# Kernel optimization log

Hardware: AMD Instinct MI355X
Metric: run time of the kernel (lower is better)

Reference implementation:

```python
import jax, jax.numpy as jnp
import numpy as np

NT, NP, E, H, DIM = 100000, 50000, 800000, 128, 128


def _lin(key, fi, fo):
    k1, k2 = jax.random.split(key)
    w = jax.random.normal(k1, (fi, fo), jnp.float32) * 0.02
    b = jax.random.normal(k2, (fo,), jnp.float32) * 0.02
    return w, b


def _conv_params(key, d_src, d_dst, d_out):
    ks = jax.random.split(key, 5)
    Wq, bq = _lin(ks[0], d_dst, d_out)
    Wk, bk = _lin(ks[1], d_src, d_out)
    Wv, bv = _lin(ks[2], d_src, d_out)
    Ws, bs = _lin(ks[3], d_dst, d_out)
    Wb = jax.random.normal(ks[4], (3 * d_out, 1), jnp.float32) * 0.02
    return Wq, bq, Wk, bk, Wv, bv, Ws, bs, Wb


def setup_inputs() -> dict:
    key = jax.random.key(0)
    ks = jax.random.split(key, 12)
    inp = {}
    inp['x_token'] = jax.random.normal(ks[0], (NT, 1), jnp.float32)
    inp['x_phrase'] = jax.random.normal(ks[1], (NP, H), jnp.float32)
    inp['W_emb'], inp['b_emb'] = _lin(ks[2], 1, H)
    (inp['Wq_tp'], inp['bq_tp'], inp['Wk_tp'], inp['bk_tp'], inp['Wv_tp'],
     inp['bv_tp'], inp['Ws_tp'], inp['bs_tp'], inp['Wb_tp']) = _conv_params(ks[3], H, H, H)
    (inp['Wq_pt'], inp['bq_pt'], inp['Wk_pt'], inp['bk_pt'], inp['Wv_pt'],
     inp['bv_pt'], inp['Ws_pt'], inp['bs_pt'], inp['Wb_pt']) = _conv_params(ks[4], H, H, H)
    inp['W_head'], inp['b_head'] = _lin(ks[5], H, DIM)
    inp['src_tp'] = jax.random.randint(ks[6], (E,), 0, NT, jnp.int32)
    inp['dst_tp'] = jax.random.randint(ks[7], (E,), 0, NP, jnp.int32)
    inp['src_pt'] = jax.random.randint(ks[8], (E,), 0, NP, jnp.int32)
    inp['dst_pt'] = jax.random.randint(ks[9], (E,), 0, NT, jnp.int32)
    return inp


def _tconv(x_src, x_dst, src, dst, Wq, bq, Wk, bk, Wv, bv, Ws, bs, Wb):
    # PyG TransformerConv, heads=1, beta=True, eval mode (no dropout).
    n_dst = x_dst.shape[0]
    d = Wq.shape[1]
    q = x_dst @ Wq + bq          # [Ndst, d]
    k = x_src @ Wk + bk          # [Nsrc, d]
    v = x_src @ Wv + bv          # [Nsrc, d]
    scores = jnp.sum(q[dst] * k[src], axis=-1) / jnp.sqrt(jnp.float32(d))  # [E]
    m = jax.ops.segment_max(scores, dst, num_segments=n_dst)
    m = jnp.where(jnp.isfinite(m), m, 0.0)  # nodes with no in-edges
    e = jnp.exp(scores - m[dst])
    denom = jax.ops.segment_sum(e, dst, num_segments=n_dst)
    alpha = e / (denom[dst] + 1e-16)                       # segment softmax over dst
    out = jax.ops.segment_sum(alpha[:, None] * v[src], dst, num_segments=n_dst)
    skip = x_dst @ Ws + bs
    beta = jax.nn.sigmoid(jnp.concatenate([out, skip, out - skip], axis=-1) @ Wb)
    return beta * skip + (1.0 - beta) * out


def _forward(x_token, x_phrase, W_emb, b_emb,
             Wq_tp, bq_tp, Wk_tp, bk_tp, Wv_tp, bv_tp, Ws_tp, bs_tp, Wb_tp,
             Wq_pt, bq_pt, Wk_pt, bk_pt, Wv_pt, bv_pt, Ws_pt, bs_pt, Wb_pt,
             W_head, b_head, src_tp, dst_tp, src_pt, dst_pt):
    h_t = x_token @ W_emb + b_emb   # [NT, H]
    h_p = x_phrase                  # [NP, H]
    # conv1 (HeteroConv aggr='sum'; each node type has exactly one incoming edge type)
    p1 = _tconv(h_t, h_p, src_tp, dst_tp, Wq_tp, bq_tp, Wk_tp, bk_tp, Wv_tp, bv_tp, Ws_tp, bs_tp, Wb_tp)
    t1 = _tconv(h_p, h_t, src_pt, dst_pt, Wq_pt, bq_pt, Wk_pt, bk_pt, Wv_pt, bv_pt, Ws_pt, bs_pt, Wb_pt)
    p1 = jax.nn.leaky_relu(p1, 0.01)
    t1 = jax.nn.leaky_relu(t1, 0.01)
    # conv2 shares the SAME conv modules (same params). Only the token output is used downstream.
    t2 = _tconv(p1, t1, src_pt, dst_pt, Wq_pt, bq_pt, Wk_pt, bk_pt, Wv_pt, bv_pt, Ws_pt, bs_pt, Wb_pt)
    return t2 @ W_head + b_head     # [NT, DIM]


def reference(x_token, x_phrase, W_emb, b_emb, Wq_tp, bq_tp, Wk_tp, bk_tp, Wv_tp, bv_tp, Ws_tp, bs_tp, Wb_tp, Wq_pt, bq_pt, Wk_pt, bk_pt, Wv_pt, bv_pt, Ws_pt, bs_pt, Wb_pt, W_head, b_head, src_tp, dst_tp, src_pt, dst_pt):
    return _forward(x_token, x_phrase, W_emb, b_emb,
                    Wq_tp, bq_tp, Wk_tp, bk_tp, Wv_tp, bv_tp, Ws_tp, bs_tp, Wb_tp,
                    Wq_pt, bq_pt, Wk_pt, bk_pt, Wv_pt, bv_pt, Ws_pt, bs_pt, Wb_pt,
                    W_head, b_head, src_tp, dst_tp, src_pt, dst_pt)
```

## Files before the change

kernel.cpp:

```cpp
#include <hip/hip_runtime.h>
#include <math.h>

#define NT 100000
#define NP 50000
#define NE 800000
#define H 128
#define NB 196
#define BCAP 8192

#define CDIV(a,b) (((a)+(b)-1)/(b))

typedef __attribute__((ext_vector_type(8))) short s16x8;
typedef __attribute__((ext_vector_type(4))) short s16x4;
typedef __attribute__((ext_vector_type(4))) unsigned short u16x4;
typedef __attribute__((ext_vector_type(4))) float f32x4;

static __device__ __forceinline__ float dot4(float4 a, float4 b){
  return a.x*b.x + a.y*b.y + a.z*b.z + a.w*b.w;
}
static __device__ __forceinline__ float b2f(unsigned short u){
  union { unsigned int i; float f; } c; c.i = ((unsigned int)u) << 16; return c.f;
}
static __device__ __forceinline__ unsigned short f2b(float f){
  union { float f; unsigned int i; } c; c.f = f;
  unsigned int x = c.i;
  unsigned int r = (x + 0x7fffu + ((x >> 16) & 1u)) >> 16;
  return (unsigned short)r;
}
static __device__ __forceinline__ float4 cvt4u(u16x4 h){
  return make_float4(b2f(h[0]), b2f(h[1]), b2f(h[2]), b2f(h[3]));
}

__global__ void kvec4(const float* __restrict__ e, const float* __restrict__ be,
    const float* W0, const float* bi0, float* u0, float* w0,
    const float* W1, const float* bi1, float* u1, float* w1,
    const float* W2, const float* bi2, float* u2, float* w2,
    const float* W3, const float* bi3, float* u3, float* w3){
  const float *W, *bi; float *u, *w;
  switch (blockIdx.x){
    case 0: W=W0; bi=bi0; u=u0; w=w0; break;
    case 1: W=W1; bi=bi1; u=u1; w=w1; break;
    case 2: W=W2; bi=bi2; u=u2; w=w2; break;
    default:W=W3; bi=bi3; u=u3; w=w3; break;
  }
  int j = threadIdx.x;
  float su = 0.f, sw = 0.f;
  for (int i = 0; i < H; ++i) {
    float wv = W[i*H + j];
    su += e[i]*wv;
    sw += be[i]*wv;
  }
  u[j] = su;
  w[j] = sw + bi[j];
}

__global__ void ksetup(const float* __restrict__ Wq, const float* __restrict__ Wk,
                       const float* __restrict__ bq, float* __restrict__ Wqk,
                       float* __restrict__ bqk){
  int i = blockIdx.x;
  int m = threadIdx.x;
  __shared__ float wqr[H];
  wqr[m] = Wq[i*H + m];
  __syncthreads();
  const float* wkr = Wk + m*H;
  float s = 0.f;
  for (int j = 0; j < H; ++j) s += wqr[j] * wkr[j];
  Wqk[i*H + m] = s;
  if (i == 0){
    float t = 0.f;
    for (int j = 0; j < H; ++j) t += bq[j] * wkr[j];
    bqk[m] = t;
  }
}
__global__ void kvqb(const float* __restrict__ Wq, const float* __restrict__ bq,
                     const float* __restrict__ bk, float* __restrict__ vqb,
                     float* __restrict__ c0){
  int i = threadIdx.x;
  float s = 0.f;
  for (int j = 0; j < H; ++j) s += Wq[i*H + j]*bk[j];
  vqb[i] = s;
  if (i == 0){
    float t = 0.f;
    for (int j = 0; j < H; ++j) t += bq[j]*bk[j];
    *c0 = t;
  }
}

__global__ void kprep(const float* W0, unsigned short* P0,
                      const float* W1, unsigned short* P1,
                      const float* W2, unsigned short* P2,
                      const float* W3, unsigned short* P3,
                      const float* W4, unsigned short* P4,
                      const float* W5, unsigned short* P5,
                      const float* W6, unsigned short* P6){
  const float* W; unsigned short* P;
  switch (blockIdx.x){
    case 0: W=W0; P=P0; break;
    case 1: W=W1; P=P1; break;
    case 2: W=W2; P=P2; break;
    case 3: W=W3; P=P3; break;
    case 4: W=W4; P=P4; break;
    case 5: W=W5; P=P5; break;
    default:W=W6; P=P6; break;
  }
  int tid = threadIdx.x;
  for (int it = 0; it < 16; ++it){
    int gid = it*256 + tid;
    int n  = gid & 127;
    int kg = gid >> 7;
    int k0 = kg*4;
    float w0 = W[(k0+0)*H + n];
    float w1 = W[(k0+1)*H + n];
    float w2 = W[(k0+2)*H + n];
    float w3 = W[(k0+3)*H + n];
    unsigned short h0=f2b(w0), h1=f2b(w1), h2=f2b(w2), h3=f2b(w3);
    s16x4 hv; hv[0]=(short)h0; hv[1]=(short)h1; hv[2]=(short)h2; hv[3]=(short)h3;
    s16x4 lv; lv[0]=(short)f2b(w0-b2f(h0)); lv[1]=(short)f2b(w1-b2f(h1));
              lv[2]=(short)f2b(w2-b2f(h2)); lv[3]=(short)f2b(w3-b2f(h3));
    int base = n*128 + (((kg>>1) ^ (n&15))<<3) + ((kg&1)<<2);
    *(s16x4*)(P + base) = hv;
    *(s16x4*)(P + 16384 + base) = lv;
  }
}

static __device__ __forceinline__ void stage_pre(const unsigned short* __restrict__ Wpre,
    unsigned short* __restrict__ WHL, int tid){
  const s16x8* src = (const s16x8*)Wpre;
  #pragma unroll
  for (int c = 0; c < 2; ++c){
    s16x8 tmp[8];
    #pragma unroll
    for (int it = 0; it < 8; ++it) tmp[it] = src[(c*8+it)*256 + tid];
    #pragma unroll
    for (int it = 0; it < 8; ++it) *(s16x8*)(WHL + ((c*8+it)*256 + tid)*8) = tmp[it];
  }
}
static __device__ __forceinline__ void stage_pre32(const unsigned short* __restrict__ Wpre,
    unsigned short* __restrict__ WH, int tid){
  const s16x8* src = (const s16x8*)Wpre;
  s16x8 tmp[8];
  #pragma unroll
  for (int it = 0; it < 8; ++it) tmp[it] = src[it*256 + tid];
  #pragma unroll
  for (int it = 0; it < 8; ++it) *(s16x8*)(WH + (it*256 + tid)*8) = tmp[it];
}

template<bool USE_AL>
static __device__ __forceinline__ void mfma_pass(const s16x8 AH[2][4], const s16x8 AL[2][4],
    const unsigned short* __restrict__ WH, const unsigned short* __restrict__ WL,
    int l15, int l4, f32x4 acc[2][8]){
  #pragma unroll
  for (int g = 0; g < 2; ++g)
    #pragma unroll
    for (int t = 0; t < 8; ++t){ acc[g][t][0]=0.f; acc[g][t][1]=0.f; acc[g][t][2]=0.f; acc[g][t][3]=0.f; }
  #pragma unroll
  for (int s = 0; s < 4; ++s){
    #pragma unroll
    for (int t = 0; t < 8; ++t){
      int n = t*16 + l15;
      int off = n*128 + (((s*4 + l4) ^ l15)<<3);
      s16x8 BH = *(const s16x8*)(WH + off);
      s16x8 BL = *(const s16x8*)(WL + off);
      #pragma unroll
      for (int g = 0; g < 2; ++g){
        acc[g][t] = __builtin_amdgcn_mfma_f32_16x16x32_bf16(AH[g][s], BH, acc[g][t], 0,0,0);
        acc[g][t] = __builtin_amdgcn_mfma_f32_16x16x32_bf16(AH[g][s], BL, acc[g][t], 0,0,0);
        if constexpr (USE_AL)
          acc[g][t] = __builtin_amdgcn_mfma_f32_16x16x32_bf16(AL[g][s], BH, acc[g][t], 0,0,0);
      }
    }
  }
}
static __device__ __forceinline__ void mfma_pass1(const s16x8 AH[2][4],
    const unsigned short* __restrict__ WH, int l15, int l4, f32x4 acc[2][8]){
  #pragma unroll
  for (int g = 0; g < 2; ++g)
    #pragma unroll
    for (int t = 0; t < 8; ++t){ acc[g][t][0]=0.f; acc[g][t][1]=0.f; acc[g][t][2]=0.f; acc[g][t][3]=0.f; }
  #pragma unroll
  for (int s = 0; s < 4; ++s){
    #pragma unroll
    for (int t = 0; t < 8; ++t){
      int n = t*16 + l15;
      int off = n*128 + (((s*4 + l4) ^ l15)<<3);
      s16x8 BH = *(const s16x8*)(WH + off);
      #pragma unroll
      for (int g = 0; g < 2; ++g)
        acc[g][t] = __builtin_amdgcn_mfma_f32_16x16x32_bf16(AH[g][s], BH, acc[g][t], 0,0,0);
    }
  }
}

static __device__ __forceinline__ void load_a_f32(const float* __restrict__ X, int M,
    int row0, int w, int l15, int l4, s16x8 AH[2][4], s16x8 AL[2][4]){
  #pragma unroll
  for (int g = 0; g < 2; ++g){
    int row = row0 + w*32 + g*16 + l15;
    const float* xr = X + (size_t)row*H;
    bool ok = row < M;
    #pragma unroll
    for (int s = 0; s < 4; ++s){
      int kb = s*32 + l4*8;
      float4 f0 = ok ? *(const float4*)(xr+kb)   : make_float4(0.f,0.f,0.f,0.f);
      float4 f1 = ok ? *(const float4*)(xr+kb+4) : make_float4(0.f,0.f,0.f,0.f);
      float xs[8] = {f0.x,f0.y,f0.z,f0.w,f1.x,f1.y,f1.z,f1.w};
      s16x8 h, lo;
      #pragma unroll
      for (int e = 0; e < 8; ++e){
        unsigned short hh = f2b(xs[e]);
        h[e]  = (short)hh;
        lo[e] = (short)f2b(xs[e] - b2f(hh));
      }
      AH[g][s] = h; AL[g][s] = lo;
    }
  }
}
static __device__ __forceinline__ void load_a_bf16(const unsigned short* __restrict__ Xb, int M,
    int row0, int w, int l15, int l4, s16x8 AH[2][4]){
  #pragma unroll
  for (int g = 0; g < 2; ++g){
    int row = row0 + w*32 + g*16 + l15;
    const unsigned short* xr = Xb + (size_t)row*H;
    bool ok = row < M;
    #pragma unroll
    for (int s = 0; s < 4; ++s){
      s16x8 h = {0,0,0,0,0,0,0,0};
      if (ok) h = *(const s16x8*)(xr + s*32 + l4*8);
      AH[g][s] = h;
    }
  }
}

static __device__ __forceinline__ void dots_epi(const f32x4 (&acc)[2][8],
    const float* __restrict__ bias, const float* __restrict__ uvec,
    const float* __restrict__ wvec, float2* __restrict__ acout,
    int row0, int M, int w, int l15, int l4){
  float ub[8], wb[8], bb[8];
  #pragma unroll
  for (int t=0;t<8;++t){ ub[t]=uvec[t*16+l15]; wb[t]=wvec[t*16+l15]; bb[t]=bias[t*16+l15]; }
  #pragma unroll
  for (int g=0; g<2; ++g){
    #pragma unroll
    for (int r=0;r<4;++r){
      float pa=0.f, pc=0.f;
      #pragma unroll
      for (int t=0;t<8;++t){ float y=acc[g][t][r]+bb[t]; pa+=y*ub[t]; pc+=y*wb[t]; }
      #pragma unroll
      for (int o=1;o<16;o<<=1){ pa+=__shfl_xor(pa,o); pc+=__shfl_xor(pc,o); }
      int row=row0+w*32+g*16+l4*4+r;
      if (l15==0 && row<M) acout[row]=make_float2(pa,pc);
    }
  }
}

static __device__ __forceinline__ void store_c_bf16(unsigned short* __restrict__ Y, int ld, int of,
    const f32x4 (&acc)[2][8], const float* __restrict__ bias,
    int row0, int M, int w, int l15, int l4){
  float bb[8];
  #pragma unroll
  for (int t=0;t<8;++t) bb[t]=bias[t*16+l15];
  #pragma unroll
  for (int g=0; g<2; ++g){
    #pragma unroll
    for (int r=0;r<4;++r){
      int row = row0 + w*32 + g*16 + l4*4 + r;
      if (row < M){
        unsigned short* dr = Y + (size_t)row*ld + of;
        #pragma unroll
        for (int t=0;t<8;++t) dr[t*16+l15] = f2b(acc[g][t][r] + bb[t]);
      }
    }
  }
}
static __device__ __forceinline__ void store_c_f32(float* __restrict__ Y,
    const f32x4 (&acc)[2][8], const float* __restrict__ bias,
    int row0, int M, int w, int l15, int l4){
  float bb[8];
  #pragma unroll
  for (int t=0;t<8;++t) bb[t]=bias[t*16+l15];
  #pragma unroll
  for (int g=0; g<2; ++g){
    #pragma unroll
    for (int r=0;r<4;++r){
      int row = row0 + w*32 + g*16 + l4*4 + r;
      if (row < M){
        float* dr = Y + (size_t)row*H;
        #pragma unroll
        for (int t=0;t<8;++t) dr[t*16+l15] = acc[g][t][r] + bb[t];
      }
    }
  }
}

__launch_bounds__(256)
__global__ void k_ph(const float* __restrict__ X, int M,
    const unsigned short* __restrict__ WqP, const float* __restrict__ bq,
    const float* __restrict__ uk, const float* __restrict__ wk, float2* __restrict__ ac1,
    const unsigned short* __restrict__ WsP, const float* __restrict__ bs, unsigned short* __restrict__ S1b,
    const unsigned short* __restrict__ WkP, const float* __restrict__ bk,
    const float* __restrict__ uq, const float* __restrict__ wq, float2* __restrict__ ac2,
    const unsigned short* __restrict__ WvP, const float* __restrict__ bv, unsigned short* __restrict__ Vb){
  __shared__ __align__(16) unsigned short WHL[32768];
  int tid=threadIdx.x, lane=tid&63, w=tid>>6, l15=lane&15, l4=lane>>4;
  int row0 = blockIdx.x*128;

  s16x8 AH[2][4], AL[2][4];
  load_a_f32(X, M, row0, w, l15, l4, AH, AL);

  f32x4 acc[2][8];
  stage_pre(WqP, WHL, tid); __syncthreads();
  mfma_pass<true>(AH, AL, WHL, WHL+16384, l15, l4, acc);
  __syncthreads();
  dots_epi(acc, bq, uk, wk, ac1, row0, M, w, l15, l4);

  stage_pre(WsP, WHL, tid); __syncthreads();
  mfma_pass<true>(AH, AL, WHL, WHL+16384, l15, l4, acc);
  __syncthreads();
  store_c_bf16(S1b, H, 0, acc, bs, row0, M, w, l15, l4);

  stage_pre(WkP, WHL, tid); __syncthreads();
  mfma_pass<true>(AH, AL, WHL, WHL+16384, l15, l4, acc);
  __syncthreads();
  dots_epi(acc, bk, uq, wq, ac2, row0, M, w, l15, l4);

  stage_pre(WvP, WHL, tid); __syncthreads();
  mfma_pass<true>(AH, AL, WHL, WHL+16384, l15, l4, acc);
  store_c_bf16(Vb, H, 0, acc, bv, row0, M, w, l15, l4);
}

__launch_bounds__(256)
__global__ void k_t3(const unsigned short* __restrict__ T1b, int M,
    const unsigned short* __restrict__ WqkP, const float* __restrict__ bqk,
    unsigned short* __restrict__ qkb,
    const float* __restrict__ vqb, const float* __restrict__ c0,
    float* __restrict__ qbf,
    const unsigned short* __restrict__ WsP, const float* __restrict__ bs,
    unsigned short* __restrict__ Sb){
  __shared__ __align__(16) unsigned short WH[16384];
  int tid=threadIdx.x, lane=tid&63, w=tid>>6, l15=lane&15, l4=lane>>4;
  int row0 = blockIdx.x*128;

  s16x8 AH[2][4];
  load_a_bf16(T1b, M, row0, w, l15, l4, AH);

  float cc0 = *c0;
  #pragma unroll
  for (int g = 0; g < 2; ++g){
    float p = 0.f;
    #pragma unroll
    for (int s = 0; s < 4; ++s){
      #pragma unroll
      for (int e = 0; e < 8; ++e)
        p += b2f((unsigned short)AH[g][s][e]) * vqb[s*32 + l4*8 + e];
    }
    p += __shfl_xor(p, 16);
    p += __shfl_xor(p, 32);
    int row = row0 + w*32 + g*16 + l15;
    if (l4 == 0 && row < M) qbf[row] = p + cc0;
  }

  f32x4 acc[2][8];
  stage_pre32(WqkP, WH, tid); __syncthreads();
  mfma_pass1(AH, WH, l15, l4, acc);
  __syncthreads();
  store_c_bf16(qkb, H, 0, acc, bqk, row0, M, w, l15, l4);

  stage_pre32(WsP, WH, tid); __syncthreads();
  mfma_pass1(AH, WH, l15, l4, acc);
  store_c_bf16(Sb, H, 0, acc, bs, row0, M, w, l15, l4);
}

__launch_bounds__(256)
__global__ void k_cmbh(const unsigned short* __restrict__ Opre, int M,
    const unsigned short* __restrict__ PV2, const float* __restrict__ bv,
    const unsigned short* __restrict__ Sb, const float* __restrict__ Wb,
    const int* __restrict__ deg,
    const unsigned short* __restrict__ PHD, const float* __restrict__ bh,
    float* __restrict__ out){
  __shared__ __align__(16) unsigned short WH[16384];
  __shared__ __align__(16) unsigned short SLDS[128][136];
  int tid=threadIdx.x, lane=tid&63, w=tid>>6, l15=lane&15, l4=lane>>4;
  int row0 = blockIdx.x*128;

  s16x8 AH[2][4];
  load_a_bf16(Opre, M, row0, w, l15, l4, AH);

  stage_pre32(PV2, WH, tid); __syncthreads();
  f32x4 acc[2][8];
  mfma_pass1(AH, WH, l15, l4, acc);

  {
    float bvv[8], wbA[8], wbB[8], wbC[8];
    #pragma unroll
    for (int t = 0; t < 8; ++t){
      int col = t*16 + l15;
      bvv[t] = bv[col];
      wbA[t] = Wb[col]; wbB[t] = Wb[H + col]; wbC[t] = Wb[2*H + col];
    }
    #pragma unroll
    for (int g = 0; g < 2; ++g){
      #pragma unroll
      for (int r = 0; r < 4; ++r){
        int rl = w*32 + g*16 + l4*4 + r;
        int row = row0 + rl;
        bool ok = row < M;
        float bsc = (ok && deg[row] > 0) ? 1.f : 0.f;
        const unsigned short* sr = Sb + (size_t)(ok ? row : 0)*H;
        float o[8], sk[8];
        float part = 0.f;
        #pragma unroll
        for (int t = 0; t < 8; ++t){
          o[t] = acc[g][t][r] + bvv[t]*bsc;
          sk[t] = ok ? b2f(sr[t*16 + l15]) : 0.f;
          part += o[t]*wbA[t] + sk[t]*wbB[t] + (o[t]-sk[t])*wbC[t];
        }
        #pragma unroll
        for (int of = 1; of < 16; of <<= 1) part += __shfl_xor(part, of);
        float beta = 1.f/(1.f + __expf(-part));
        #pragma unroll
        for (int t = 0; t < 8; ++t){
          float vv = beta*sk[t] + (1.f-beta)*o[t];
          SLDS[rl][t*16 + l15] = f2b(vv);
        }
      }
    }
  }
  __syncthreads();

  s16x8 A2[2][4];
  #pragma unroll
  for (int g = 0; g < 2; ++g){
    int rl = w*32 + g*16 + l15;
    #pragma unroll
    for (int s = 0; s < 4; ++s)
      A2[g][s] = *(const s16x8*)&SLDS[rl][s*32 + l4*8];
  }
  stage_pre32(PHD, WH, tid);
  __syncthreads();

  f32x4 a2[2][8];
  mfma_pass1(A2, WH, l15, l4, a2);
  store_c_f32(out, a2, bh, row0, M, w, l15, l4);
}

template<int GATHER>
__launch_bounds__(256)
__global__ void passA(const int* __restrict__ dst, const int* __restrict__ src,
                      const float* __restrict__ xv, int shift,
                      int* __restrict__ bcnt, int2* __restrict__ out, int n){
  __shared__ int hist[NB];
  __shared__ int base[NB];
  __shared__ int cur[NB];
  int tid = threadIdx.x;
  for (int i = tid; i < NB; i += 256){ hist[i]=0; cur[i]=0; }
  __syncthreads();
  int e0 = blockIdx.x*2048;
  int d[8], s[8];
  #pragma unroll
  for (int k = 0; k < 8; ++k){
    int i = e0 + k*256 + tid;
    if (i < n){ d[k] = dst[i]; s[k] = src[i]; }
    else d[k] = -1;
  }
  #pragma unroll
  for (int k = 0; k < 8; ++k)
    if (d[k] >= 0) atomicAdd(&hist[d[k]>>shift], 1);
  __syncthreads();
  for (int b = tid; b < NB; b += 256)
    base[b] = hist[b] ? atomicAdd(&bcnt[b], hist[b]) : 0;
  __syncthreads();
  #pragma unroll
  for (int k = 0; k < 8; ++k){
    if (d[k] >= 0){
      int b = d[k] >> shift;
      int loc = atomicAdd(&cur[b], 1);
      int2 rec;
      if constexpr (GATHER) rec.x = __float_as_int(xv[s[k]]);
      else                  rec.x = s[k];
      rec.y = d[k] - (b << shift);
      out[(size_t)b*BCAP + base[b] + loc] = rec;
    }
  }
}

__launch_bounds__(512)
__global__ void passB_ph(const int* __restrict__ bcnt, const int2* __restrict__ sorted,
                         const float2* __restrict__ ac, float2* __restrict__ dsv, int np){
  __shared__ float2 acl[256];
  __shared__ float accx[256];
  __shared__ float accy[256];
  int b = blockIdx.x, tid = threadIdx.x;
  int p0 = b*256;
  if (tid < 256){
    int p = p0 + tid;
    acl[tid] = (p < np) ? ac[p] : make_float2(0.f,0.f);
    accx[tid] = 0.f; accy[tid] = 0.f;
  }
  __syncthreads();
  int n = bcnt[b];
  const int2* e = sorted + (size_t)b*BCAP;
  const float RS = 0.08838834764831845f;
  for (int i = tid; i < n; i += 512){
    int2 ed = e[i];
    float x = __int_as_float(ed.x);
    float2 a = acl[ed.y];
    float ex = __expf((x*a.x + a.y)*RS);
    atomicAdd(&accx[ed.y], ex);
    atomicAdd(&accy[ed.y], ex*x);
  }
  __syncthreads();
  if (tid < 256){
    int p = p0 + tid;
    if (p < np) dsv[p] = make_float2(accx[tid], accy[tid]);
  }
}

__launch_bounds__(512)
__global__ void passB_tok(const int* __restrict__ bcnt, const int2* __restrict__ sorted,
                          int* __restrict__ rowptr, int* __restrict__ deg,
                          int* __restrict__ srcs, int ntok){
  __shared__ int cnt[512];
  __shared__ int scn[512];
  __shared__ int cur[512];
  int b = blockIdx.x, tid = threadIdx.x;
  cnt[tid] = 0; cur[tid] = 0;
  __syncthreads();
  int n = bcnt[b];
  const int2* e = sorted + (size_t)b*BCAP;
  for (int i = tid; i < n; i += 512) atomicAdd(&cnt[e[i].y], 1);
  __syncthreads();
  int myc = cnt[tid];
  scn[tid] = myc;
  __syncthreads();
  for (int off = 1; off < 512; off <<= 1){
    int u = (tid >= off) ? scn[tid-off] : 0;
    __syncthreads();
    scn[tid] += u;
    __syncthreads();
  }
  int excl = scn[tid] - myc;
  int tok = b*512 + tid;
  if (tok < ntok){ rowptr[tok] = b*BCAP + excl; deg[tok] = myc; }
  __syncthreads();
  cnt[tid] = excl;
  __syncthreads();
  for (int i = tid; i < n; i += 512){
    int2 ed = e[i];
    int pos = cnt[ed.y] + atomicAdd(&cur[ed.y], 1);
    srcs[(size_t)b*BCAP + pos] = ed.x;
  }
}

template<int OB>
static __device__ __forceinline__ void beta_combine(float4 o, float4 sk,
    const float* __restrict__ Wb, int lane, bool leaky, void* __restrict__ dstRow){
  float4 wb0 = *(const float4*)&Wb[lane*4];
  float4 wb1 = *(const float4*)&Wb[H   + lane*4];
  float4 wb2 = *(const float4*)&Wb[2*H + lane*4];
  float4 dv = make_float4(o.x-sk.x, o.y-sk.y, o.z-sk.z, o.w-sk.w);
  float part = dot4(o,wb0) + dot4(sk,wb1) + dot4(dv,wb2);
  #pragma unroll
  for (int off=1; off<32; off<<=1) part += __shfl_xor(part, off);
  float beta = 1.f/(1.f + __expf(-part));
  float4 r;
  r.x = beta*sk.x + (1.f-beta)*o.x;
  r.y = beta*sk.y + (1.f-beta)*o.y;
  r.z = beta*sk.z + (1.f-beta)*o.z;
  r.w = beta*sk.w + (1.f-beta)*o.w;
  if (leaky){
    r.x = r.x>0.f? r.x : 0.01f*r.x;
    r.y = r.y>0.f? r.y : 0.01f*r.y;
    r.z = r.z>0.f? r.z : 0.01f*r.z;
    r.w = r.w>0.f? r.w : 0.01f*r.w;
  }
  if constexpr (OB){
    ushort4 h; h.x=f2b(r.x); h.y=f2b(r.y); h.z=f2b(r.z); h.w=f2b(r.w);
    *(ushort4*)((unsigned short*)dstRow + lane*4) = h;
  } else {
    *(float4*)((float*)dstRow + lane*4) = r;
  }
}

static __device__ __forceinline__ void beta_combine16(const float o[8], const float sk[8],
    const float* __restrict__ Wb, int lane, bool leaky, unsigned short* __restrict__ dstRow){
  float part = 0.f;
  #pragma unroll
  for (int e = 0; e < 8; ++e){
    int col = lane*8 + e;
    part += o[e]*Wb[col] + sk[e]*Wb[H+col] + (o[e]-sk[e])*Wb[2*H+col];
  }
  #pragma unroll
  for (int off = 1; off < 16; off <<= 1) part += __shfl_xor(part, off);
  float beta = 1.f/(1.f + __expf(-part));
  s16x8 h;
  #pragma unroll
  for (int e = 0; e < 8; ++e){
    float r = beta*sk[e] + (1.f-beta)*o[e];
    if (leaky) r = r > 0.f ? r : 0.01f*r;
    h[e] = (short)f2b(r);
  }
  *(s16x8*)(dstRow + lane*8) = h;
}

__global__ void kcomb1(const float2* __restrict__ dsv,
                       const float* __restrict__ uv, const float* __restrict__ wv,
                       const unsigned short* __restrict__ S, const float* __restrict__ Wb,
                       unsigned short* __restrict__ out, int n){
  int gid = (blockIdx.x*blockDim.x + threadIdx.x) >> 5;
  int lane = threadIdx.x & 31;
  if (gid >= n) return;
  float2 ds = dsv[gid];
  float d = ds.x, sv = ds.y;
  float inv = 1.f/(d + 1e-16f);
  float4 u4 = *(const float4*)&uv[lane*4];
  float4 w4 = *(const float4*)&wv[lane*4];
  float4 o = make_float4((sv*u4.x + d*w4.x)*inv, (sv*u4.y + d*w4.y)*inv,
                         (sv*u4.z + d*w4.z)*inv, (sv*u4.w + d*w4.w)*inv);
  u16x4 sh4 = __builtin_nontemporal_load((const u16x4*)(S + (size_t)gid*H + lane*4));
  float4 sk = cvt4u(sh4);
  beta_combine<1>(o, sk, Wb, lane, true, out + (size_t)gid*H);
}

__global__ void knode2(const float* __restrict__ x_tok, const float2* __restrict__ ac,
                       const unsigned short* __restrict__ Vb,
                       const int* __restrict__ rowptr, const int* __restrict__ deg,
                       const int* __restrict__ srcs,
                       const float* __restrict__ us, const float* __restrict__ ws,
                       const float* __restrict__ Wb, unsigned short* __restrict__ out, int n){
  int gid = (blockIdx.x*blockDim.x + threadIdx.x) >> 4;
  int lane = threadIdx.x & 15;
  if (gid >= n) return;
  float xt = x_tok[gid];
  int rp = rowptr[gid], dg = deg[gid];
  const float RS = 0.08838834764831845f;
  float d = 0.f;
  float acc[8] = {0.f,0.f,0.f,0.f,0.f,0.f,0.f,0.f};
  int i = 0;
  for (; i+2 <= dg; i += 2){
    int spA = srcs[rp+i], spB = srcs[rp+i+1];
    s16x8 hA = *(const s16x8*)(Vb + (size_t)spA*H + lane*8);
    s16x8 hB = *(const s16x8*)(Vb + (size_t)spB*H + lane*8);
    float2 aA = ac[spA], aB = ac[spB];
    float eA = __expf((xt*aA.x + aA.y)*RS);
    float eB = __expf((xt*aB.x + aB.y)*RS);
    d += eA + eB;
    #pragma unroll
    for (int e = 0; e < 8; ++e)
      acc[e] += eA*b2f((unsigned short)hA[e]) + eB*b2f((unsigned short)hB[e]);
  }
  if (i < dg){
    int sp = srcs[rp+i];
    s16x8 hv = *(const s16x8*)(Vb + (size_t)sp*H + lane*8);
    float2 a = ac[sp];
    float ex = __expf((xt*a.x + a.y)*RS);
    d += ex;
    #pragma unroll
    for (int e = 0; e < 8; ++e) acc[e] += ex*b2f((unsigned short)hv[e]);
  }
  float inv = 1.f/(d + 1e-16f);
  float o[8], sk[8];
  #pragma unroll
  for (int e = 0; e < 8; ++e){
    int col = lane*8 + e;
    o[e]  = acc[e]*inv;
    sk[e] = xt*us[col] + ws[col];
  }
  beta_combine16(o, sk, Wb, lane, true, out + (size_t)gid*H);
}

__global__ void knode3n(const unsigned short* __restrict__ qkb, const float* __restrict__ qbf,
                        const unsigned short* __restrict__ P1b,
                        const int* __restrict__ rowptr, const int* __restrict__ deg,
                        const int* __restrict__ srcs,
                        unsigned short* __restrict__ Opre, int n){
  int gid = (blockIdx.x*blockDim.x + threadIdx.x) >> 4;
  int lane = threadIdx.x & 15;
  if (gid >= n) return;
  float q[8];
  {
    s16x8 qh = *(const s16x8*)(qkb + (size_t)gid*H + lane*8);
    #pragma unroll
    for (int e = 0; e < 8; ++e) q[e] = b2f((unsigned short)qh[e]);
  }
  float qb = qbf[gid];
  int rp = rowptr[gid], dg = deg[gid];
  const float RS = 0.08838834764831845f;
  float d = 0.f;
  float acc[8] = {0.f,0.f,0.f,0.f,0.f,0.f,0.f,0.f};
  int i = 0;
  for (; i+2 <= dg; i += 2){
    int spA = srcs[rp+i], spB = srcs[rp+i+1];
    s16x8 hA = *(const s16x8*)(P1b + (size_t)spA*H + lane*8);
    s16x8 hB = *(const s16x8*)(P1b + (size_t)spB*H + lane*8);
    float pA[8], pB[8];
    float psA = 0.f, psB = 0.f;
    #pragma unroll
    for (int e = 0; e < 8; ++e){
      pA[e] = b2f((unsigned short)hA[e]);
      pB[e] = b2f((unsigned short)hB[e]);
      psA += q[e]*pA[e];
      psB += q[e]*pB[e];
    }
    #pragma unroll
    for (int off=1; off<16; off<<=1){ psA += __shfl_xor(psA,off); psB += __shfl_xor(psB,off); }
    float eA = __expf((psA + qb)*RS), eB = __expf((psB + qb)*RS);
    d += eA + eB;
    #pragma unroll
    for (int e = 0; e < 8; ++e) acc[e] += eA*pA[e] + eB*pB[e];
  }
  if (i < dg){
    int sp = srcs[rp+i];
    s16x8 h = *(const s16x8*)(P1b + (size_t)sp*H + lane*8);
    float p[8];
    float ps = 0.f;
    #pragma unroll
    for (int e = 0; e < 8; ++e){ p[e] = b2f((unsigned short)h[e]); ps += q[e]*p[e]; }
    #pragma unroll
    for (int off=1; off<16; off<<=1) ps += __shfl_xor(ps,off);
    float ex = __expf((ps + qb)*RS);
    d += ex;
    #pragma unroll
    for (int e = 0; e < 8; ++e) acc[e] += ex*p[e];
  }
  float inv = 1.f/(d + 1e-16f);
  s16x8 hres;
  #pragma unroll
  for (int e = 0; e < 8; ++e) hres[e] = (short)f2b(acc[e]*inv);
  *(s16x8*)(Opre + (size_t)gid*H + lane*8) = hres;
}

extern "C" void kernel_launch(void* const* d_in, const int* in_sizes, int n_in,
                              void* d_out, int out_size, void* d_ws, size_t ws_size,
                              hipStream_t stream){
  const float* x_token  = (const float*)d_in[0];
  const float* x_phrase = (const float*)d_in[1];
  const float* W_emb    = (const float*)d_in[2];
  const float* b_emb    = (const float*)d_in[3];
  const float* Wq_tp = (const float*)d_in[4];  const float* bq_tp = (const float*)d_in[5];
  const float* Wk_tp = (const float*)d_in[6];  const float* bk_tp = (const float*)d_in[7];
  const float* Wv_tp = (const float*)d_in[8];  const float* bv_tp = (const float*)d_in[9];
  const float* Ws_tp = (const float*)d_in[10]; const float* bs_tp = (const float*)d_in[11];
  const float* Wb_tp = (const float*)d_in[12];
  const float* Wq_pt = (const float*)d_in[13]; const float* bq_pt = (const float*)d_in[14];
  const float* Wk_pt = (const float*)d_in[15]; const float* bk_pt = (const float*)d_in[16];
  const float* Wv_pt = (const float*)d_in[17]; const float* bv_pt = (const float*)d_in[18];
  const float* Ws_pt = (const float*)d_in[19]; const float* bs_pt = (const float*)d_in[20];
  const float* Wb_pt = (const float*)d_in[21];
  const float* W_head = (const float*)d_in[22]; const float* b_head = (const float*)d_in[23];
  const int* src_tp = (const int*)d_in[24];
  const int* dst_tp = (const int*)d_in[25];
  const int* src_pt = (const int*)d_in[26];
  const int* dst_pt = (const int*)d_in[27];
  float* out = (float*)d_out;

  char* base = (char*)d_ws;
  size_t off = 0;
  auto AB = [&](size_t bytes)->void*{ void* p=(void*)(base+off); off += (bytes+15)&~(size_t)15; return p; };
  unsigned short* S1b = (unsigned short*)AB((size_t)NP*H*2);
  unsigned short* P1b = (unsigned short*)AB((size_t)NP*H*2);
  unsigned short* VQ  = (unsigned short*)AB((size_t)NT*H*2);
  unsigned short* Sb  = (unsigned short*)AB((size_t)NT*H*2);
  unsigned short* T1b = (unsigned short*)AB((size_t)NT*H*2);
  unsigned short* qkb = (unsigned short*)AB((size_t)NT*H*2);
  unsigned short* Vb   = VQ;
  unsigned short* Opre = VQ;
  float* qbf = (float*)AB((size_t)NT*4);
  float* Wqk = (float*)AB((size_t)H*H*4);
  float* bqk = (float*)AB((size_t)H*4);
  float* vqb = (float*)AB((size_t)H*4);
  float* c0  = (float*)AB(16);
  unsigned short* PQ1 = (unsigned short*)AB(32768*2);
  unsigned short* PS1 = (unsigned short*)AB(32768*2);
  unsigned short* PK2 = (unsigned short*)AB(32768*2);
  unsigned short* PV2 = (unsigned short*)AB(32768*2);
  unsigned short* PS3 = (unsigned short*)AB(32768*2);
  unsigned short* PHD = (unsigned short*)AB(32768*2);
  unsigned short* PQK = (unsigned short*)AB(32768*2);
  float* vecs = (float*)AB(8*H*4);
  float* uk1=vecs, *wk1=vecs+H, *uv1=vecs+2*H, *wv1=vecs+3*H;
  float* uq2=vecs+4*H, *wq2=vecs+5*H, *us2=vecs+6*H, *ws2=vecs+7*H;
  float2* ac1  = (float2*)AB((size_t)NP*8);
  float2* ac2  = (float2*)AB((size_t)NP*8);
  float2* dsv2 = (float2*)AB((size_t)NP*8);
  int2* sortedP = (int2*)AB((size_t)NB*BCAP*8);
  int2* sortedT = (int2*)AB((size_t)NB*BCAP*8);
  int*  srcsT   = (int*)AB((size_t)NB*BCAP*4);
  int* rowT = (int*)AB((size_t)NT*4);
  int* degT = (int*)AB((size_t)NT*4);
  int* bcnt = (int*)AB((size_t)2*NB*4);
  int* bcntP = bcnt, * bcntT = bcnt + NB;
  (void)ws_size; (void)in_sizes; (void)n_in; (void)out_size;

  const int gP = CDIV(NP,128), gT = CDIV(NT,128);
  const int nbA = CDIV(NE,2048);

  kvec4<<<4,H,0,stream>>>(W_emb, b_emb,
      Wk_tp, bk_tp, uk1, wk1,
      Wv_tp, bv_tp, uv1, wv1,
      Wq_pt, bq_pt, uq2, wq2,
      Ws_pt, bs_pt, us2, ws2);
  ksetup<<<H,H,0,stream>>>(Wq_pt, Wk_pt, bq_pt, Wqk, bqk);
  kvqb<<<1,H,0,stream>>>(Wq_pt, bq_pt, bk_pt, vqb, c0);
  kprep<<<7,256,0,stream>>>(Wq_tp, PQ1, Ws_tp, PS1, Wk_pt, PK2, Wv_pt, PV2,
                            Ws_pt, PS3, W_head, PHD, Wqk, PQK);

  (void)hipMemsetAsync(bcnt, 0, (size_t)2*NB*4, stream);
  passA<1><<<nbA,256,0,stream>>>(dst_tp, src_tp, x_token, 8, bcntP, sortedP, NE);
  passA<0><<<nbA,256,0,stream>>>(dst_pt, src_pt, nullptr, 9, bcntT, sortedT, NE);
  passB_tok<<<NB,512,0,stream>>>(bcntT, sortedT, rowT, degT, srcsT, NT);

  k_ph<<<gP,256,0,stream>>>(x_phrase, NP,
      PQ1, bq_tp, uk1, wk1, ac1,
      PS1, bs_tp, S1b,
      PK2, bk_pt, uq2, wq2, ac2,
      PV2, bv_pt, Vb);

  passB_ph<<<NB,512,0,stream>>>(bcntP, sortedP, ac1, dsv2, NP);
  kcomb1<<<CDIV(NP*32,256),256,0,stream>>>(dsv2, uv1, wv1, S1b, Wb_tp, P1b, NP);

  knode2<<<CDIV(NT*16,256),256,0,stream>>>(x_token, ac2, Vb, rowT, degT, srcsT,
                                           us2, ws2, Wb_pt, T1b, NT);

  k_t3<<<gT,256,0,stream>>>(T1b, NT, PQK, bqk, qkb, vqb, c0, qbf,
                            PS3, bs_pt, Sb);
  knode3n<<<CDIV(NT*16,256),256,0,stream>>>(qkb, qbf, P1b, rowT, degT, srcsT,
                                            Opre, NT);
  k_cmbh<<<gT,256,0,stream>>>(Opre, NT, PV2, bv_pt, Sb, Wb_pt, degT,
                              PHD, b_head, out);
}
```

Baseline: 282.8 us.

## Use 512-thread blocks with 16 rows per wave in dense MFMA kernels

The three dense GEMM kernels (k_ph, k_t3, k_cmbh) move from 256 threads with 32 rows per wave to 512 threads with 16 rows per wave, keeping 128 rows per block. Each wave now holds half as many A fragments and accumulators, which cuts register pressure and should raise occupancy and latency hiding. Weight staging into LDS is spread over twice as many threads. In exchange, each B fragment read from LDS feeds only one row group instead of two, so LDS traffic per MFMA doubles.

After: 269.9 us. -4.5%, faster.

```diff
diff --git a/kernel.cpp b/kernel.cpp
--- a/kernel.cpp
+++ b/kernel.cpp
@@ -123,36 +123,31 @@
   }
 }
 
-static __device__ __forceinline__ void stage_pre(const unsigned short* __restrict__ Wpre,
+static __device__ __forceinline__ void stage_pre64_512(const unsigned short* __restrict__ Wpre,
     unsigned short* __restrict__ WHL, int tid){
   const s16x8* src = (const s16x8*)Wpre;
-  #pragma unroll
-  for (int c = 0; c < 2; ++c){
-    s16x8 tmp[8];
-    #pragma unroll
-    for (int it = 0; it < 8; ++it) tmp[it] = src[(c*8+it)*256 + tid];
-    #pragma unroll
-    for (int it = 0; it < 8; ++it) *(s16x8*)(WHL + ((c*8+it)*256 + tid)*8) = tmp[it];
-  }
-}
-static __device__ __forceinline__ void stage_pre32(const unsigned short* __restrict__ Wpre,
+  s16x8 tmp[8];
+  #pragma unroll
+  for (int it = 0; it < 8; ++it) tmp[it] = src[it*512 + tid];
+  #pragma unroll
+  for (int it = 0; it < 8; ++it) *(s16x8*)(WHL + (it*512 + tid)*8) = tmp[it];
+}
+static __device__ __forceinline__ void stage_pre32_512(const unsigned short* __restrict__ Wpre,
     unsigned short* __restrict__ WH, int tid){
   const s16x8* src = (const s16x8*)Wpre;
-  s16x8 tmp[8];
-  #pragma unroll
-  for (int it = 0; it < 8; ++it) tmp[it] = src[it*256 + tid];
-  #pragma unroll
-  for (int it = 0; it < 8; ++it) *(s16x8*)(WH + (it*256 + tid)*8) = tmp[it];
+  s16x8 tmp[4];
+  #pragma unroll
+  for (int it = 0; it < 4; ++it) tmp[it] = src[it*512 + tid];
+  #pragma unroll
+  for (int it = 0; it < 4; ++it) *(s16x8*)(WH + (it*512 + tid)*8) = tmp[it];
 }
 
 template<bool USE_AL>
-static __device__ __forceinline__ void mfma_pass(const s16x8 AH[2][4], const s16x8 AL[2][4],
+static __device__ __forceinline__ void mfma_passW(const s16x8 AH[4], const s16x8 AL[4],
     const unsigned short* __restrict__ WH, const unsigned short* __restrict__ WL,
-    int l15, int l4, f32x4 acc[2][8]){
-  #pragma unroll
-  for (int g = 0; g < 2; ++g)
-    #pragma unroll
-    for (int t = 0; t < 8; ++t){ acc[g][t][0]=0.f; acc[g][t][1]=0.f; acc[g][t][2]=0.f; acc[g][t][3]=0.f; }
+    int l15, int l4, f32x4 acc[8]){
+  #pragma unroll
+  for (int t = 0; t < 8; ++t){ acc[t][0]=0.f; acc[t][1]=0.f; acc[t][2]=0.f; acc[t][3]=0.f; }
   #pragma unroll
   for (int s = 0; s < 4; ++s){
     #pragma unroll
@@ -161,22 +156,17 @@
       int off = n*128 + (((s*4 + l4) ^ l15)<<3);
       s16x8 BH = *(const s16x8*)(WH + off);
       s16x8 BL = *(const s16x8*)(WL + off);
-      #pragma unroll
-      for (int g = 0; g < 2; ++g){
-        acc[g][t] = __builtin_amdgcn_mfma_f32_16x16x32_bf16(AH[g][s], BH, acc[g][t], 0,0,0);
-        acc[g][t] = __builtin_amdgcn_mfma_f32_16x16x32_bf16(AH[g][s], BL, acc[g][t], 0,0,0);
-        if constexpr (USE_AL)
-          acc[g][t] = __builtin_amdgcn_mfma_f32_16x16x32_bf16(AL[g][s], BH, acc[g][t], 0,0,0);
-      }
-    }
-  }
-}
-static __device__ __forceinline__ void mfma_pass1(const s16x8 AH[2][4],
-    const unsigned short* __restrict__ WH, int l15, int l4, f32x4 acc[2][8]){
-  #pragma unroll
-  for (int g = 0; g < 2; ++g)
-    #pragma unroll
-    for (int t = 0; t < 8; ++t){ acc[g][t][0]=0.f; acc[g][t][1]=0.f; acc[g][t][2]=0.f; acc[g][t][3]=0.f; }
+      acc[t] = __builtin_amdgcn_mfma_f32_16x16x32_bf16(AH[s], BH, acc[t], 0,0,0);
+      acc[t] = __builtin_amdgcn_mfma_f32_16x16x32_bf16(AH[s], BL, acc[t], 0,0,0);
+      if constexpr (USE_AL)
+        acc[t] = __builtin_amdgcn_mfma_f32_16x16x32_bf16(AL[s], BH, acc[t], 0,0,0);
+    }
+  }
+}
+static __device__ __forceinline__ void mfma_passW1(const s16x8 AH[4],
+    const unsigned short* __restrict__ WH, int l15, int l4, f32x4 acc[8]){
+  #pragma unroll
+  for (int t = 0; t < 8; ++t){ acc[t][0]=0.f; acc[t][1]=0.f; acc[t][2]=0.f; acc[t][3]=0.f; }
   #pragma unroll
   for (int s = 0; s < 4; ++s){
     #pragma unroll
@@ -184,115 +174,98 @@
       int n = t*16 + l15;
       int off = n*128 + (((s*4 + l4) ^ l15)<<3);
       s16x8 BH = *(const s16x8*)(WH + off);
-      #pragma unroll
-      for (int g = 0; g < 2; ++g)
-        acc[g][t] = __builtin_amdgcn_mfma_f32_16x16x32_bf16(AH[g][s], BH, acc[g][t], 0,0,0);
-    }
-  }
-}
-
-static __device__ __forceinline__ void load_a_f32(const float* __restrict__ X, int M,
-    int row0, int w, int l15, int l4, s16x8 AH[2][4], s16x8 AL[2][4]){
-  #pragma unroll
-  for (int g = 0; g < 2; ++g){
-    int row = row0 + w*32 + g*16 + l15;
-    const float* xr = X + (size_t)row*H;
-    bool ok = row < M;
-    #pragma unroll
-    for (int s = 0; s < 4; ++s){
-      int kb = s*32 + l4*8;
-      float4 f0 = ok ? *(const float4*)(xr+kb)   : make_float4(0.f,0.f,0.f,0.f);
-      float4 f1 = ok ? *(const float4*)(xr+kb+4) : make_float4(0.f,0.f,0.f,0.f);
-      float xs[8] = {f0.x,f0.y,f0.z,f0.w,f1.x,f1.y,f1.z,f1.w};
-      s16x8 h, lo;
-      #pragma unroll
-      for (int e = 0; e < 8; ++e){
-        unsigned short hh = f2b(xs[e]);
-        h[e]  = (short)hh;
-        lo[e] = (short)f2b(xs[e] - b2f(hh));
-      }
-      AH[g][s] = h; AL[g][s] = lo;
-    }
-  }
-}
-static __device__ __forceinline__ void load_a_bf16(const unsigned short* __restrict__ Xb, int M,
-    int row0, int w, int l15, int l4, s16x8 AH[2][4]){
-  #pragma unroll
-  for (int g = 0; g < 2; ++g){
-    int row = row0 + w*32 + g*16 + l15;
-    const unsigned short* xr = Xb + (size_t)row*H;
-    bool ok = row < M;
-    #pragma unroll
-    for (int s = 0; s < 4; ++s){
-      s16x8 h = {0,0,0,0,0,0,0,0};
-      if (ok) h = *(const s16x8*)(xr + s*32 + l4*8);
-      AH[g][s] = h;
-    }
-  }
-}
-
-static __device__ __forceinline__ void dots_epi(const f32x4 (&acc)[2][8],
+      acc[t] = __builtin_amdgcn_mfma_f32_16x16x32_bf16(AH[s], BH, acc[t], 0,0,0);
+    }
+  }
+}
+
+static __device__ __forceinline__ void load_aw_f32(const float* __restrict__ X, int M,
+    int rowb, int l15, int l4, s16x8 AH[4], s16x8 AL[4]){
+  int row = rowb + l15;
+  const float* xr = X + (size_t)row*H;
+  bool ok = row < M;
+  #pragma unroll
+  for (int s = 0; s < 4; ++s){
+    int kb = s*32 + l4*8;
+    float4 f0 = ok ? *(const float4*)(xr+kb)   : make_float4(0.f,0.f,0.f,0.f);
+    float4 f1 = ok ? *(const float4*)(xr+kb+4) : make_float4(0.f,0.f,0.f,0.f);
+    float xs[8] = {f0.x,f0.y,f0.z,f0.w,f1.x,f1.y,f1.z,f1.w};
+    s16x8 h, lo;
+    #pragma unroll
+    for (int e = 0; e < 8; ++e){
+      unsigned short hh = f2b(xs[e]);
+      h[e]  = (short)hh;
+      lo[e] = (short)f2b(xs[e] - b2f(hh));
+    }
+    AH[s] = h; AL[s] = lo;
+  }
+}
+static __device__ __forceinline__ void load_aw_bf16(const unsigned short* __restrict__ Xb, int M,
+    int rowb, int l15, int l4, s16x8 AH[4]){
+  int row = rowb + l15;
+  const unsigned short* xr = Xb + (size_t)row*H;
+  bool ok = row < M;
+  #pragma unroll
+  for (int s = 0; s < 4; ++s){
+    s16x8 h = {0,0,0,0,0,0,0,0};
+    if (ok) h = *(const s16x8*)(xr + s*32 + l4*8);
+    AH[s] = h;
+  }
+}
+
+static __device__ __forceinline__ void dots_epiW(const f32x4 (&acc)[8],
     const float* __restrict__ bias, const float* __restrict__ uvec,
     const float* __restrict__ wvec, float2* __restrict__ acout,
-    int row0, int M, int w, int l15, int l4){
+    int rowb, int M, int l15, int l4){
   float ub[8], wb[8], bb[8];
   #pragma unroll
   for (int t=0;t<8;++t){ ub[t]=uvec[t*16+l15]; wb[t]=wvec[t*16+l15]; bb[t]=bias[t*16+l15]; }
   #pragma unroll
-  for (int g=0; g<2; ++g){
-    #pragma unroll
-    for (int r=0;r<4;++r){
-      float pa=0.f, pc=0.f;
+  for (int r=0;r<4;++r){
+    float pa=0.f, pc=0.f;
+    #pragma unroll
+    for (int t=0;t<8;++t){ float y=acc[t][r]+bb[t]; pa+=y*ub[t]; pc+=y*wb[t]; }
+    #pragma unroll
+    for (int o=1;o<16;o<<=1){ pa+=__shfl_xor(pa,o); pc+=__shfl_xor(pc,o); }
+    int row = rowb + l4*4 + r;
+    if (l15==0 && row<M) acout[row]=make_float2(pa,pc);
+  }
+}
+
+static __device__ __forceinline__ void store_cw_bf16(unsigned short* __restrict__ Y,
+    const f32x4 (&acc)[8], const float* __restrict__ bias,
+    int rowb, int M, int l15, int l4){
+  float bb[8];
+  #pragma unroll
+  for (int t=0;t<8;++t) bb[t]=bias[t*16+l15];
+  #pragma unroll
+  for (int r=0;r<4;++r){
+    int row = rowb + l4*4 + r;
+    if (row < M){
+      unsigned short* dr = Y + (size_t)row*H;
       #pragma unroll
-      for (int t=0;t<8;++t){ float y=acc[g][t][r]+bb[t]; pa+=y*ub[t]; pc+=y*wb[t]; }
+      for (int t=0;t<8;++t) dr[t*16+l15] = f2b(acc[t][r] + bb[t]);
+    }
+  }
+}
+static __device__ __forceinline__ void store_cw_f32(float* __restrict__ Y,
+    const f32x4 (&acc)[8], const float* __restrict__ bias,
+    int rowb, int M, int l15, int l4){
+  float bb[8];
+  #pragma unroll
+  for (int t=0;t<8;++t) bb[t]=bias[t*16+l15];
+  #pragma unroll
+  for (int r=0;r<4;++r){
+    int row = rowb + l4*4 + r;
+    if (row < M){
+      float* dr = Y + (size_t)row*H;
       #pragma unroll
-      for (int o=1;o<16;o<<=1){ pa+=__shfl_xor(pa,o); pc+=__shfl_xor(pc,o); }
-      int row=row0+w*32+g*16+l4*4+r;
-      if (l15==0 && row<M) acout[row]=make_float2(pa,pc);
-    }
-  }
-}
-
-static __device__ __forceinline__ void store_c_bf16(unsigned short* __restrict__ Y, int ld, int of,
-    const f32x4 (&acc)[2][8], const float* __restrict__ bias,
-    int row0, int M, int w, int l15, int l4){
-  float bb[8];
-  #pragma unroll
-  for (int t=0;t<8;++t) bb[t]=bias[t*16+l15];
-  #pragma unroll
-  for (int g=0; g<2; ++g){
-    #pragma unroll
-    for (int r=0;r<4;++r){
-      int row = row0 + w*32 + g*16 + l4*4 + r;
-      if (row < M){
-        unsigned short* dr = Y + (size_t)row*ld + of;
-        #pragma unroll
-        for (int t=0;t<8;++t) dr[t*16+l15] = f2b(acc[g][t][r] + bb[t]);
-      }
-    }
-  }
-}
-static __device__ __forceinline__ void store_c_f32(float* __restrict__ Y,
-    const f32x4 (&acc)[2][8], const float* __restrict__ bias,
-    int row0, int M, int w, int l15, int l4){
-  float bb[8];
-  #pragma unroll
-  for (int t=0;t<8;++t) bb[t]=bias[t*16+l15];
-  #pragma unroll
-  for (int g=0; g<2; ++g){
-    #pragma unroll
-    for (int r=0;r<4;++r){
-      int row = row0 + w*32 + g*16 + l4*4 + r;
-      if (row < M){
-        float* dr = Y + (size_t)row*H;
-        #pragma unroll
-        for (int t=0;t<8;++t) dr[t*16+l15] = acc[g][t][r] + bb[t];
-      }
-    }
-  }
-}
-
-__launch_bounds__(256)
+      for (int t=0;t<8;++t) dr[t*16+l15] = acc[t][r] + bb[t];
+    }
+  }
+}
+
+__launch_bounds__(512)
 __global__ void k_ph(const float* __restrict__ X, int M,
     const unsigned short* __restrict__ WqP, const float* __restrict__ bq,
     const float* __restrict__ uk, const float* __restrict__ wk, float2* __restrict__ ac1,
@@ -302,33 +275,33 @@
     const unsigned short* __restrict__ WvP, const float* __restrict__ bv, unsigned short* __restrict__ Vb){
   __shared__ __align__(16) unsigned short WHL[32768];
   int tid=threadIdx.x, lane=tid&63, w=tid>>6, l15=lane&15, l4=lane>>4;
-  int row0 = blockIdx.x*128;
-
-  s16x8 AH[2][4], AL[2][4];
-  load_a_f32(X, M, row0, w, l15, l4, AH, AL);
-
-  f32x4 acc[2][8];
-  stage_pre(WqP, WHL, tid); __syncthreads();
-  mfma_pass<true>(AH, AL, WHL, WHL+16384, l15, l4, acc);
-  __syncthreads();
-  dots_epi(acc, bq, uk, wk, ac1, row0, M, w, l15, l4);
-
-  stage_pre(WsP, WHL, tid); __syncthreads();
-  mfma_pass<true>(AH, AL, WHL, WHL+16384, l15, l4, acc);
-  __syncthreads();
-  store_c_bf16(S1b, H, 0, acc, bs, row0, M, w, l15, l4);
-
-  stage_pre(WkP, WHL, tid); __syncthreads();
-  mfma_pass<true>(AH, AL, WHL, WHL+16384, l15, l4, acc);
-  __syncthreads();
-  dots_epi(acc, bk, uq, wq, ac2, row0, M, w, l15, l4);
-
-  stage_pre(WvP, WHL, tid); __syncthreads();
-  mfma_pass<true>(AH, AL, WHL, WHL+16384, l15, l4, acc);
-  store_c_bf16(Vb, H, 0, acc, bv, row0, M, w, l15, l4);
-}
-
-__launch_bounds__(256)
+  int rowb = blockIdx.x*128 + w*16;
+
+  s16x8 AH[4], AL[4];
+  load_aw_f32(X, M, rowb, l15, l4, AH, AL);
+
+  f32x4 acc[8];
+  stage_pre64_512(WqP, WHL, tid); __syncthreads();
+  mfma_passW<true>(AH, AL, WHL, WHL+16384, l15, l4, acc);
+  __syncthreads();
+  dots_epiW(acc, bq, uk, wk, ac1, rowb, M, l15, l4);
+
+  stage_pre64_512(WsP, WHL, tid); __syncthreads();
+  mfma_passW<true>(AH, AL, WHL, WHL+16384, l15, l4, acc);
+  __syncthreads();
+  store_cw_bf16(S1b, acc, bs, rowb, M, l15, l4);
+
+  stage_pre64_512(WkP, WHL, tid); __syncthreads();
+  mfma_passW<true>(AH, AL, WHL, WHL+16384, l15, l4, acc);
+  __syncthreads();
+  dots_epiW(acc, bk, uq, wq, ac2, rowb, M, l15, l4);
+
+  stage_pre64_512(WvP, WHL, tid); __syncthreads();
+  mfma_passW<true>(AH, AL, WHL, WHL+16384, l15, l4, acc);
+  store_cw_bf16(Vb, acc, bv, rowb, M, l15, l4);
+}
+
+__launch_bounds__(512)
 __global__ void k_t3(const unsigned short* __restrict__ T1b, int M,
     const unsigned short* __restrict__ WqkP, const float* __restrict__ bqk,
     unsigned short* __restrict__ qkb,
@@ -338,39 +311,38 @@
     unsigned short* __restrict__ Sb){
   __shared__ __align__(16) unsigned short WH[16384];
   int tid=threadIdx.x, lane=tid&63, w=tid>>6, l15=lane&15, l4=lane>>4;
-  int row0 = blockIdx.x*128;
-
-  s16x8 AH[2][4];
-  load_a_bf16(T1b, M, row0, w, l15, l4, AH);
+  int rowb = blockIdx.x*128 + w*16;
+
+  s16x8 AH[4];
+  load_aw_bf16(T1b, M, rowb, l15, l4, AH);
 
   float cc0 = *c0;
-  #pragma unroll
-  for (int g = 0; g < 2; ++g){
+  {
     float p = 0.f;
     #pragma unroll
     for (int s = 0; s < 4; ++s){
       #pragma unroll
       for (int e = 0; e < 8; ++e)
-        p += b2f((unsigned short)AH[g][s][e]) * vqb[s*32 + l4*8 + e];
+        p += b2f((unsigned short)AH[s][e]) * vqb[s*32 + l4*8 + e];
     }
     p += __shfl_xor(p, 16);
     p += __shfl_xor(p, 32);
-    int row = row0 + w*32 + g*16 + l15;
+    int row = rowb + l15;
     if (l4 == 0 && row < M) qbf[row] = p + cc0;
   }
 
-  f32x4 acc[2][8];
-  stage_pre32(WqkP, WH, tid); __syncthreads();
-  mfma_pass1(AH, WH, l15, l4, acc);
-  __syncthreads();
-  store_c_bf16(qkb, H, 0, acc, bqk, row0, M, w, l15, l4);
-
-  stage_pre32(WsP, WH, tid); __syncthreads();
-  mfma_pass1(AH, WH, l15, l4, acc);
-  store_c_bf16(Sb, H, 0, acc, bs, row0, M, w, l15, l4);
-}
-
-__launch_bounds__(256)
+  f32x4 acc[8];
+  stage_pre32_512(WqkP, WH, tid); __syncthreads();
+  mfma_passW1(AH, WH, l15, l4, acc);
+  __syncthreads();
+  store_cw_bf16(qkb, acc, bqk, rowb, M, l15, l4);
+
+  stage_pre32_512(WsP, WH, tid); __syncthreads();
+  mfma_passW1(AH, WH, l15, l4, acc);
+  store_cw_bf16(Sb, acc, bs, rowb, M, l15, l4);
+}
+
+__launch_bounds__(512)
 __global__ void k_cmbh(const unsigned short* __restrict__ Opre, int M,
     const unsigned short* __restrict__ PV2, const float* __restrict__ bv,
     const unsigned short* __restrict__ Sb, const float* __restrict__ Wb,
@@ -381,13 +353,14 @@
   __shared__ __align__(16) unsigned short SLDS[128][136];
   int tid=threadIdx.x, lane=tid&63, w=tid>>6, l15=lane&15, l4=lane>>4;
   int row0 = blockIdx.x*128;
-
-  s16x8 AH[2][4];
-  load_a_bf16(Opre, M, row0, w, l15, l4, AH);
-
-  stage_pre32(PV2, WH, tid); __syncthreads();
-  f32x4 acc[2][8];
-  mfma_pass1(AH, WH, l15, l4, acc);
+  int rowb = row0 + w*16;
+
+  s16x8 AH[4];
+  load_aw_bf16(Opre, M, rowb, l15, l4, AH);
+
+  stage_pre32_512(PV2, WH, tid); __syncthreads();
+  f32x4 acc[8];
+  mfma_passW1(AH, WH, l15, l4, acc);
 
   {
     float bvv[8], wbA[8], wbB[8], wbC[8];
@@ -398,49 +371,45 @@
       wbA[t] = Wb[col]; wbB[t] = Wb[H + col]; wbC[t] = Wb[2*H + col];
     }
     #pragma unroll
-    for (int g = 0; g < 2; ++g){
+    for (int r = 0; r < 4; ++r){
+      int rl = w*16 + l4*4 + r;
+      int row = row0 + rl;
+      bool ok = row < M;
+      float bsc = (ok && deg[row] > 0) ? 1.f : 0.f;
+      const unsigned short* sr = Sb + (size_t)(ok ? row : 0)*H;
+      float o[8], sk[8];
+      float part = 0.f;
       #pragma unroll
-      for (int r = 0; r < 4; ++r){
-        int rl = w*32 + g*16 + l4*4 + r;
-        int row = row0 + rl;
-        bool ok = row < M;
-        float bsc = (ok && deg[row] > 0) ? 1.f : 0.f;
-        const unsigned short* sr = Sb + (size_t)(ok ? row : 0)*H;
-        float o[8], sk[8];
-        float part = 0.f;
-        #pragma unroll
-        for (int t = 0; t < 8; ++t){
-          o[t] = acc[g][t][r] + bvv[t]*bsc;
-          sk[t] = ok ? b2f(sr[t*16 + l15]) : 0.f;
-          part += o[t]*wbA[t] + sk[t]*wbB[t] + (o[t]-sk[t])*wbC[t];
-        }
-        #pragma unroll
-        for (int of = 1; of < 16; of <<= 1) part += __shfl_xor(part, of);
-        float beta = 1.f/(1.f + __expf(-part));
-        #pragma unroll
-        for (int t = 0; t < 8; ++t){
-          float vv = beta*sk[t] + (1.f-beta)*o[t];
-          SLDS[rl][t*16 + l15] = f2b(vv);
-        }
+      for (int t = 0; t < 8; ++t){
+        o[t] = acc[t][r] + bvv[t]*bsc;
+        sk[t] = ok ? b2f(sr[t*16 + l15]) : 0.f;
+        part += o[t]*wbA[t] + sk[t]*wbB[t] + (o[t]-sk[t])*wbC[t];
       }
-    }
-  }
-  __syncthreads();
-
-  s16x8 A2[2][4];
-  #pragma unroll
-  for (int g = 0; g < 2; ++g){
-    int rl = w*32 + g*16 + l15;
+      #pragma unroll
+      for (int of = 1; of < 16; of <<= 1) part += __shfl_xor(part, of);
+      float beta = 1.f/(1.f + __expf(-part));
+      #pragma unroll
+      for (int t = 0; t < 8; ++t){
+        float vv = beta*sk[t] + (1.f-beta)*o[t];
+        SLDS[rl][t*16 + l15] = f2b(vv);
+      }
+    }
+  }
+  __syncthreads();
+
+  s16x8 A2[4];
+  {
+    int rl = w*16 + l15;
     #pragma unroll
     for (int s = 0; s < 4; ++s)
-      A2[g][s] = *(const s16x8*)&SLDS[rl][s*32 + l4*8];
-  }
-  stage_pre32(PHD, WH, tid);
-  __syncthreads();
-
-  f32x4 a2[2][8];
-  mfma_pass1(A2, WH, l15, l4, a2);
-  store_c_f32(out, a2, bh, row0, M, w, l15, l4);
+      A2[s] = *(const s16x8*)&SLDS[rl][s*32 + l4*8];
+  }
+  stage_pre32_512(PHD, WH, tid);
+  __syncthreads();
+
+  f32x4 a2[8];
+  mfma_passW1(A2, WH, l15, l4, a2);
+  store_cw_f32(out, a2, bh, rowb, M, l15, l4);
 }
 
 template<int GATHER>
@@ -809,7 +778,7 @@
   passA<0><<<nbA,256,0,stream>>>(dst_pt, src_pt, nullptr, 9, bcntT, sortedT, NE);
   passB_tok<<<NB,512,0,stream>>>(bcntT, sortedT, rowT, degT, srcsT, NT);
 
-  k_ph<<<gP,256,0,stream>>>(x_phrase, NP,
+  k_ph<<<gP,512,0,stream>>>(x_phrase, NP,
       PQ1, bq_tp, uk1, wk1, ac1,
       PS1, bs_tp, S1b,
       PK2, bk_pt, uq2, wq2, ac2,
@@ -821,10 +790,10 @@
   knode2<<<CDIV(NT*16,256),256,0,stream>>>(x_token, ac2, Vb, rowT, degT, srcsT,
                                            us2, ws2, Wb_pt, T1b, NT);
 
-  k_t3<<<gT,256,0,stream>>>(T1b, NT, PQK, bqk, qkb, vqb, c0, qbf,
+  k_t3<<<gT,512,0,stream>>>(T1b, NT, PQK, bqk, qkb, vqb, c0, qbf,
                             PS3, bs_pt, Sb);
   knode3n<<<CDIV(NT*16,256),256,0,stream>>>(qkb, qbf, P1b, rowT, degT, srcsT,
                                             Opre, NT);
-  k_cmbh<<<gT,256,0,stream>>>(Opre, NT, PV2, bv_pt, Sb, Wb_pt, degT,
+  k_cmbh<<<gT,512,0,stream>>>(Opre, NT, PV2, bv_pt, Sb, Wb_pt, degT,
                               PHD, b_head, out);
 }
```
